# Performance work log

Hardware: AMD Instinct MI355X
Metric: run time of the kernel (lower is better)

## Reference

```python
import jax, jax.numpy as jnp
import numpy as np

I_SZ, H_SZ, B, T = 256, 512, 32, 2048


def _lin_params(key, fan_in, out):
    kw, kb = jax.random.split(key)
    s = 1.0 / np.sqrt(fan_in)
    W = jax.random.uniform(kw, (out, fan_in), minval=-s, maxval=s, dtype=jnp.float32)
    b = jax.random.uniform(kb, (out,), minval=-s, maxval=s, dtype=jnp.float32)
    return W, b


def setup_inputs() -> dict:
    key = jax.random.key(0)
    ks = jax.random.split(key, 11)
    inp = {
        'x': jax.random.normal(ks[0], (B, T, I_SZ), dtype=jnp.float32),
        'hx': jax.random.normal(ks[1], (B, H_SZ), dtype=jnp.float32),
        'cx': jax.random.normal(ks[2], (B, H_SZ), dtype=jnp.float32),
    }
    names_in = ['Wii', 'Wif', 'Wic', 'Wio']
    names_h = ['Whi', 'Whf', 'Whc', 'Who']
    for i, n in enumerate(names_in):
        W, b = _lin_params(ks[3 + i], I_SZ, H_SZ)
        inp[n] = W
        inp['b' + n[1:]] = b
    for i, n in enumerate(names_h):
        W, b = _lin_params(ks[7 + i], H_SZ, H_SZ)
        inp[n] = W
        inp['b' + n[1:]] = b
    return inp


def reference(x, hx, cx, Wii, bii, Wif, bif, Wic, bic, Wio, bio,
              Whi, bhi, Whf, bhf, Whc, bhc, Who, bho):
    # batch_first: [B,T,I] -> [T,B,I]
    xs = jnp.swapaxes(x, 0, 1)
    t, b, _ = xs.shape
    # Fuse the 4 input-to-hidden projections over the whole sequence (same math)
    xi = jnp.einsum('tbi,hi->tbh', xs, Wii) + bii
    xf = jnp.einsum('tbi,hi->tbh', xs, Wif) + bif
    xc = jnp.einsum('tbi,hi->tbh', xs, Wic) + bic
    xo = jnp.einsum('tbi,hi->tbh', xs, Wio) + bio

    def step(carry, gates_x):
        h, c, _, _, _ = carry
        xi_t, xf_t, xc_t, xo_t = gates_x
        ig = jax.nn.sigmoid(xi_t + h @ Whi.T + bhi)
        fg = jax.nn.sigmoid(xf_t + h @ Whf.T + bhf)
        cg = jnp.tanh(xc_t + h @ Whc.T + bhc)
        og = jax.nn.sigmoid(xo_t + h @ Who.T + bho)
        cy = fg * c + ig * cg
        hy = og * jnp.tanh(cy)
        return (hy, cy, ig, fg, og), hy

    z = jnp.zeros((b, H_SZ), dtype=x.dtype)
    (hn, cn, ig_n, fg_n, og_n), ys = jax.lax.scan(
        step, (hx, cx, z, z, z), (xi, xf, xc, xo))
    # torch.cat(list of [B,H], dim=0) -> [T*B, H]; then transpose(0,1) -> [H, T*B]
    out = ys.reshape(t * b, H_SZ).T
    return (out, hn, cn, ig_n, fg_n, og_n)
```

## Files before the change

### kernel.cpp

```cpp
#include <hip/hip_runtime.h>
#include <hip/hip_bf16.h>


typedef _Float16 f16x8 __attribute__((ext_vector_type(8)));
typedef float    f32x16 __attribute__((ext_vector_type(16)));

#define NBLK   32
#define TSTEPS 2048

#define WS_WH    0
#define WS_WX    2097152
#define WS_XG    3145728
#define WS_HG    36700160
#define WS_BIAS  36765696
#define WS_CNT   36773888

#define OUT_MAIN 33554432
#define OFF_HN   (OUT_MAIN)
#define OFF_CN   (OUT_MAIN + 16384)
#define OFF_IG   (OUT_MAIN + 32768)
#define OFF_FG   (OUT_MAIN + 49152)
#define OFF_OG   (OUT_MAIN + 65536)

struct Ptrs { const float* p[16]; };

__device__ __forceinline__ float sigf(float v) {
    return 1.0f / (1.0f + __expf(-v));
}
__device__ __forceinline__ float tanhf_(float v) {
    float a = fabsf(v);
    float e = __expf(-2.0f * a);
    float r = (1.0f - e) / (1.0f + e);
    return v < 0.0f ? -r : r;
}

__global__ void setup_kernel(Ptrs P, const float* __restrict__ hx,
                             _Float16* __restrict__ WH16, _Float16* __restrict__ WX16,
                             float* __restrict__ BIAS, _Float16* __restrict__ HG,
                             unsigned* __restrict__ CNT)
{
    int idx = blockIdx.x * 256 + threadIdx.x;
    if (idx < 1048576) {
        int g = idx >> 18; int r = idx & 262143;
        WH16[idx] = (_Float16)P.p[8 + 2*g][r];
    } else if (idx < 1572864) {
        int j = idx - 1048576; int g = j >> 17; int r = j & 131071;
        WX16[j] = (_Float16)P.p[2*g][r];
    } else if (idx < 1574912) {
        int j = idx - 1572864; int g = j >> 9; int c = j & 511;
        BIAS[j] = P.p[2*g + 1][c] + P.p[8 + 2*g + 1][c];
    } else if (idx < 1576960) {
        int ch = idx - 1574912;
        int kf = ch >> 6; int lane = ch & 63;
        int b = lane & 31; int k0 = (kf*2 + (lane >> 5)) * 8;
        f16x8 o;
        #pragma unroll
        for (int e = 0; e < 8; ++e) o[e] = (_Float16)hx[b*512 + k0 + e];
        *(f16x8*)(HG + (size_t)ch * 8) = o;
    } else if (idx == 1576960) {
        *CNT = 0u;
    }
}

__global__ void xconv_kernel(const float* __restrict__ x, _Float16* __restrict__ XG)
{
    int ch = blockIdx.x * 256 + threadIdx.x;
    int t = ch >> 10; int rest = ch & 1023;
    int kf = rest >> 6; int lane = rest & 63;
    int b = lane & 31; int i0 = (kf*2 + (lane >> 5)) * 8;
    const float* src = x + ((size_t)b * 2048 + t) * 256 + i0;
    float4 u = *(const float4*)src;
    float4 v = *(const float4*)(src + 4);
    f16x8 o;
    o[0]=(_Float16)u.x; o[1]=(_Float16)u.y; o[2]=(_Float16)u.z; o[3]=(_Float16)u.w;
    o[4]=(_Float16)v.x; o[5]=(_Float16)v.y; o[6]=(_Float16)v.z; o[7]=(_Float16)v.w;
    *(f16x8*)(XG + (size_t)ch * 8) = o;
}

__global__ __launch_bounds__(256, 1) void lstm_rec(
    const float* __restrict__ cx, float* __restrict__ out,
    const _Float16* __restrict__ WH16, const _Float16* __restrict__ WX16,
    const _Float16* __restrict__ XG, _Float16* __restrict__ HG,
    const float* __restrict__ BIAS, unsigned* __restrict__ CNT)
{
    __shared__ float part[2][32][66];
    __shared__ float bias_lds[4][16];

    const int tid = threadIdx.x;
    const int bk  = blockIdx.x;
    const int jbase = bk * 16;
    const int w  = tid >> 6;
    const int l  = tid & 63;
    const int kh = w & 1;
    const int cs = w >> 1;
    const int n  = l & 31;
    const int kg = l >> 5;

    if (tid < 64) bias_lds[tid >> 4][tid & 15] = BIAS[(tid >> 4)*512 + jbase + (tid & 15)];

    const int c_loc = cs*32 + n;
    const int g  = c_loc >> 4;
    const int jr = jbase + (c_loc & 15);

    f16x8 bf[24];
    #pragma unroll
    for (int m = 0; m < 16; ++m) {
        int k = (kh*16 + m)*16 + kg*8;
        bf[m] = *(const f16x8*)(WH16 + ((size_t)g*512 + jr)*512 + k);
    }
    #pragma unroll
    for (int m = 0; m < 8; ++m) {
        int i = (kh*8 + m)*16 + kg*8;
        bf[16 + m] = *(const f16x8*)(WX16 + ((size_t)g*512 + jr)*256 + i);
    }

    const int eb = tid & 31;
    const int ej = tid >> 5;
    float c0 = cx[eb*512 + jbase + ej];
    float c1 = cx[eb*512 + jbase + ej + 8];

    __syncthreads();

    for (int t = 0; t < TSTEPS; ++t) {
        const _Float16* hcur = HG + (size_t)(t & 1) * 16384;

        f16x8 ah[16], ax[8];
        #pragma unroll
        for (int m = 0; m < 8; ++m)
            ax[m] = *(const f16x8*)(XG + (size_t)t*8192 + (size_t)(kh*8 + m)*512 + l*8);
        #pragma unroll
        for (int m = 0; m < 16; ++m)
            ah[m] = *(const f16x8*)(hcur + (size_t)(kh*16 + m)*512 + l*8);

        f32x16 accA, accB;
        #pragma unroll
        for (int i = 0; i < 16; ++i) { accA[i] = 0.0f; accB[i] = 0.0f; }

        #pragma unroll
        for (int m = 0; m < 8; m += 2) {
            accA = __builtin_amdgcn_mfma_f32_32x32x16_f16(ax[m],   bf[16+m],   accA, 0, 0, 0);
            accB = __builtin_amdgcn_mfma_f32_32x32x16_f16(ax[m+1], bf[16+m+1], accB, 0, 0, 0);
        }
        #pragma unroll
        for (int m = 0; m < 16; m += 2) {
            accA = __builtin_amdgcn_mfma_f32_32x32x16_f16(ah[m],   bf[m],   accA, 0, 0, 0);
            accB = __builtin_amdgcn_mfma_f32_32x32x16_f16(ah[m+1], bf[m+1], accB, 0, 0, 0);
        }

        #pragma unroll
        for (int r = 0; r < 16; ++r) {
            int b = (r & 3) + 8*(r >> 2) + 4*kg;
            part[kh][b][c_loc] = accA[r] + accB[r];
        }
        __syncthreads();

        _Float16* hnxt = HG + (size_t)((t + 1) & 1) * 16384;
        float hy0, hy1;
        {
            float v0 = part[0][eb][ 0 + ej] + part[1][eb][ 0 + ej] + bias_lds[0][ej];
            float v1 = part[0][eb][16 + ej] + part[1][eb][16 + ej] + bias_lds[1][ej];
            float v2 = part[0][eb][32 + ej] + part[1][eb][32 + ej] + bias_lds[2][ej];
            float v3 = part[0][eb][48 + ej] + part[1][eb][48 + ej] + bias_lds[3][ej];
            float ig = sigf(v0), fg = sigf(v1), cg = tanhf_(v2), og = sigf(v3);
            c0 = fg*c0 + ig*cg;
            hy0 = og * tanhf_(c0);
            if (t == TSTEPS - 1) {
                int k = jbase + ej;
                out[OFF_HN + eb*512 + k] = hy0;
                out[OFF_CN + eb*512 + k] = c0;
                out[OFF_IG + eb*512 + k] = ig;
                out[OFF_FG + eb*512 + k] = fg;
                out[OFF_OG + eb*512 + k] = og;
            }
        }
        {
            int ej2 = ej + 8;
            float v0 = part[0][eb][ 0 + ej2] + part[1][eb][ 0 + ej2] + bias_lds[0][ej2];
            float v1 = part[0][eb][16 + ej2] + part[1][eb][16 + ej2] + bias_lds[1][ej2];
            float v2 = part[0][eb][32 + ej2] + part[1][eb][32 + ej2] + bias_lds[2][ej2];
            float v3 = part[0][eb][48 + ej2] + part[1][eb][48 + ej2] + bias_lds[3][ej2];
            float ig = sigf(v0), fg = sigf(v1), cg = tanhf_(v2), og = sigf(v3);
            c1 = fg*c1 + ig*cg;
            hy1 = og * tanhf_(c1);
            if (t == TSTEPS - 1) {
                int k = jbase + ej2;
                out[OFF_HN + eb*512 + k] = hy1;
                out[OFF_CN + eb*512 + k] = c1;
                out[OFF_IG + eb*512 + k] = ig;
                out[OFF_FG + eb*512 + k] = fg;
                out[OFF_OG + eb*512 + k] = og;
            }
        }

        out[(size_t)(jbase + ej)     * 65536 + t*32 + eb] = hy0;
        out[(size_t)(jbase + ej + 8) * 65536 + t*32 + eb] = hy1;

        {
            int k  = jbase + ej;
            hnxt[bk*512 + eb*8 + ej]        = (_Float16)hy0;
            hnxt[bk*512 + (32 + eb)*8 + ej] = (_Float16)hy1;
            (void)k;
        }

        __syncthreads();
        if (tid == 0) {
            __threadfence();
            __hip_atomic_fetch_add(CNT, 1u, __ATOMIC_RELAXED, __HIP_MEMORY_SCOPE_AGENT);
            const unsigned tgt = (unsigned)NBLK * (unsigned)(t + 1);
            while (__hip_atomic_load(CNT, __ATOMIC_RELAXED, __HIP_MEMORY_SCOPE_AGENT) < tgt) {
                __builtin_amdgcn_s_sleep(1);
            }
            __threadfence();
        }
        __syncthreads();
    }
}

extern "C" void kernel_launch(void* const* d_in, const int* in_sizes, int n_in,
                              void* d_out, int out_size, void* d_ws, size_t ws_size,
                              hipStream_t stream)
{
    const float* x  = (const float*)d_in[0];
    const float* hx = (const float*)d_in[1];
    const float* cx = (const float*)d_in[2];

    Ptrs P;
    for (int i = 0; i < 16; ++i) P.p[i] = (const float*)d_in[3 + i];

    char* ws = (char*)d_ws;
    _Float16* WH16 = (_Float16*)(ws + WS_WH);
    _Float16* WX16 = (_Float16*)(ws + WS_WX);
    _Float16* XG   = (_Float16*)(ws + WS_XG);
    _Float16* HG   = (_Float16*)(ws + WS_HG);
    float*    BIAS = (float*)   (ws + WS_BIAS);
    unsigned* CNT  = (unsigned*)(ws + WS_CNT);

    float* out = (float*)d_out;

    setup_kernel<<<6161, 256, 0, stream>>>(P, hx, WH16, WX16, BIAS, HG, CNT);
    xconv_kernel<<<8192, 256, 0, stream>>>(x, XG);
    lstm_rec<<<NBLK, 256, 0, stream>>>(cx, out, WH16, WX16, XG, HG, BIAS, CNT);
}
```

Before: 12.97 ms.

## Replace atomic-counter grid barrier with per-block flags and overlap x-projection

Swaps the single global atomic counter barrier for per-block step flags. Each block publishes its step number after writing h, and a single wave polls all 32 flags before reading h. The input-projection MFMAs now run before the wait, and the h-vector and global output stores move after the flag publish so they overlap with other blocks' progress. h is written as packed half2 atomic stores with a changed column assignment. Correctness relies on relaxed atomics plus an explicit vmcnt wait instead of threadfences, which risks memory-ordering subtleties.

```diff
diff --git a/kernel.cpp b/kernel.cpp
--- a/kernel.cpp
+++ b/kernel.cpp
@@ -13,7 +13,7 @@
 #define WS_XG    3145728
 #define WS_HG    36700160
 #define WS_BIAS  36765696
-#define WS_CNT   36773888
+#define WS_FLG   36773888
 
 #define OUT_MAIN 33554432
 #define OFF_HN   (OUT_MAIN)
@@ -37,7 +37,7 @@
 __global__ void setup_kernel(Ptrs P, const float* __restrict__ hx,
                              _Float16* __restrict__ WH16, _Float16* __restrict__ WX16,
                              float* __restrict__ BIAS, _Float16* __restrict__ HG,
-                             unsigned* __restrict__ CNT)
+                             unsigned* __restrict__ FLAGS)
 {
     int idx = blockIdx.x * 256 + threadIdx.x;
     if (idx < 1048576) {
@@ -57,8 +57,8 @@
         #pragma unroll
         for (int e = 0; e < 8; ++e) o[e] = (_Float16)hx[b*512 + k0 + e];
         *(f16x8*)(HG + (size_t)ch * 8) = o;
-    } else if (idx == 1576960) {
-        *CNT = 0u;
+    } else if (idx < 1576992) {
+        FLAGS[idx - 1576960] = 0u;
     }
 }
 
@@ -81,7 +81,7 @@
     const float* __restrict__ cx, float* __restrict__ out,
     const _Float16* __restrict__ WH16, const _Float16* __restrict__ WX16,
     const _Float16* __restrict__ XG, _Float16* __restrict__ HG,
-    const float* __restrict__ BIAS, unsigned* __restrict__ CNT)
+    const float* __restrict__ BIAS, unsigned* __restrict__ FLAGS)
 {
     __shared__ float part[2][32][66];
     __shared__ float bias_lds[4][16];
@@ -115,22 +115,18 @@
     }
 
     const int eb = tid & 31;
-    const int ej = tid >> 5;
-    float c0 = cx[eb*512 + jbase + ej];
-    float c1 = cx[eb*512 + jbase + ej + 8];
+    const int ep = tid >> 5;
+    float c0 = cx[eb*512 + jbase + 2*ep];
+    float c1 = cx[eb*512 + jbase + 2*ep + 1];
+    const int hdw = bk*256 + (ep < 4 ? (eb*4 + ep) : ((32 + eb)*4 + (ep - 4)));
 
     __syncthreads();
 
     for (int t = 0; t < TSTEPS; ++t) {
-        const _Float16* hcur = HG + (size_t)(t & 1) * 16384;
-
-        f16x8 ah[16], ax[8];
+        f16x8 ax[8];
         #pragma unroll
         for (int m = 0; m < 8; ++m)
             ax[m] = *(const f16x8*)(XG + (size_t)t*8192 + (size_t)(kh*8 + m)*512 + l*8);
-        #pragma unroll
-        for (int m = 0; m < 16; ++m)
-            ah[m] = *(const f16x8*)(hcur + (size_t)(kh*16 + m)*512 + l*8);
 
         f32x16 accA, accB;
         #pragma unroll
@@ -141,6 +137,28 @@
             accA = __builtin_amdgcn_mfma_f32_32x32x16_f16(ax[m],   bf[16+m],   accA, 0, 0, 0);
             accB = __builtin_amdgcn_mfma_f32_32x32x16_f16(ax[m+1], bf[16+m+1], accB, 0, 0, 0);
         }
+
+        if (w == 0) {
+            for (;;) {
+                unsigned v = __hip_atomic_load(FLAGS + (l & 31), __ATOMIC_RELAXED,
+                                               __HIP_MEMORY_SCOPE_AGENT);
+                if (__all((int)(v >= (unsigned)t))) break;
+                __builtin_amdgcn_s_sleep(1);
+            }
+        }
+        __syncthreads();
+
+        const unsigned long long* hcur64 =
+            (const unsigned long long*)HG + (size_t)(t & 1) * 4096;
+        f16x8 ah[16];
+        #pragma unroll
+        for (int m = 0; m < 16; ++m) {
+            int bofs = ((kh*16 + m)*64 + l) * 2;
+            union { f16x8 v; unsigned long long u[2]; } tq;
+            tq.u[0] = __hip_atomic_load(hcur64 + bofs,     __ATOMIC_RELAXED, __HIP_MEMORY_SCOPE_AGENT);
+            tq.u[1] = __hip_atomic_load(hcur64 + bofs + 1, __ATOMIC_RELAXED, __HIP_MEMORY_SCOPE_AGENT);
+            ah[m] = tq.v;
+        }
         #pragma unroll
         for (int m = 0; m < 16; m += 2) {
             accA = __builtin_amdgcn_mfma_f32_32x32x16_f16(ah[m],   bf[m],   accA, 0, 0, 0);
@@ -154,65 +172,50 @@
         }
         __syncthreads();
 
-        _Float16* hnxt = HG + (size_t)((t + 1) & 1) * 16384;
-        float hy0, hy1;
+        const int ca = 2*ep, cb = 2*ep + 1;
+        float hy0, hy1, ig0, fg0, og0, ig1, fg1, og1;
         {
-            float v0 = part[0][eb][ 0 + ej] + part[1][eb][ 0 + ej] + bias_lds[0][ej];
-            float v1 = part[0][eb][16 + ej] + part[1][eb][16 + ej] + bias_lds[1][ej];
-            float v2 = part[0][eb][32 + ej] + part[1][eb][32 + ej] + bias_lds[2][ej];
-            float v3 = part[0][eb][48 + ej] + part[1][eb][48 + ej] + bias_lds[3][ej];
-            float ig = sigf(v0), fg = sigf(v1), cg = tanhf_(v2), og = sigf(v3);
-            c0 = fg*c0 + ig*cg;
-            hy0 = og * tanhf_(c0);
-            if (t == TSTEPS - 1) {
-                int k = jbase + ej;
-                out[OFF_HN + eb*512 + k] = hy0;
-                out[OFF_CN + eb*512 + k] = c0;
-                out[OFF_IG + eb*512 + k] = ig;
-                out[OFF_FG + eb*512 + k] = fg;
-                out[OFF_OG + eb*512 + k] = og;
-            }
+            float v0 = part[0][eb][ 0 + ca] + part[1][eb][ 0 + ca] + bias_lds[0][ca];
+            float v1 = part[0][eb][16 + ca] + part[1][eb][16 + ca] + bias_lds[1][ca];
+            float v2 = part[0][eb][32 + ca] + part[1][eb][32 + ca] + bias_lds[2][ca];
+            float v3 = part[0][eb][48 + ca] + part[1][eb][48 + ca] + bias_lds[3][ca];
+            ig0 = sigf(v0); fg0 = sigf(v1); float cg = tanhf_(v2); og0 = sigf(v3);
+            c0 = fg0*c0 + ig0*cg;
+            hy0 = og0 * tanhf_(c0);
         }
         {
-            int ej2 = ej + 8;
-            float v0 = part[0][eb][ 0 + ej2] + part[1][eb][ 0 + ej2] + bias_lds[0][ej2];
-            float v1 = part[0][eb][16 + ej2] + part[1][eb][16 + ej2] + bias_lds[1][ej2];
-            float v2 = part[0][eb][32 + ej2] + part[1][eb][32 + ej2] + bias_lds[2][ej2];
-            float v3 = part[0][eb][48 + ej2] + part[1][eb][48 + ej2] + bias_lds[3][ej2];
-            float ig = sigf(v0), fg = sigf(v1), cg = tanhf_(v2), og = sigf(v3);
-            c1 = fg*c1 + ig*cg;
-            hy1 = og * tanhf_(c1);
-            if (t == TSTEPS - 1) {
-                int k = jbase + ej2;
-                out[OFF_HN + eb*512 + k] = hy1;
-                out[OFF_CN + eb*512 + k] = c1;
-                out[OFF_IG + eb*512 + k] = ig;
-                out[OFF_FG + eb*512 + k] = fg;
-                out[OFF_OG + eb*512 + k] = og;
-            }
-        }
-
-        out[(size_t)(jbase + ej)     * 65536 + t*32 + eb] = hy0;
-        out[(size_t)(jbase + ej + 8) * 65536 + t*32 + eb] = hy1;
+            float v0 = part[0][eb][ 0 + cb] + part[1][eb][ 0 + cb] + bias_lds[0][cb];
+            float v1 = part[0][eb][16 + cb] + part[1][eb][16 + cb] + bias_lds[1][cb];
+            float v2 = part[0][eb][32 + cb] + part[1][eb][32 + cb] + bias_lds[2][cb];
+            float v3 = part[0][eb][48 + cb] + part[1][eb][48 + cb] + bias_lds[3][cb];
+            ig1 = sigf(v0); fg1 = sigf(v1); float cg = tanhf_(v2); og1 = sigf(v3);
+            c1 = fg1*c1 + ig1*cg;
+            hy1 = og1 * tanhf_(c1);
+        }
 
         {
-            int k  = jbase + ej;
-            hnxt[bk*512 + eb*8 + ej]        = (_Float16)hy0;
-            hnxt[bk*512 + (32 + eb)*8 + ej] = (_Float16)hy1;
-            (void)k;
-        }
-
+            union { unsigned u; _Float16 h[2]; } pk;
+            pk.h[0] = (_Float16)hy0; pk.h[1] = (_Float16)hy1;
+            unsigned* hnxt32 = (unsigned*)HG + (size_t)((t + 1) & 1) * 8192;
+            __hip_atomic_store(hnxt32 + hdw, pk.u, __ATOMIC_RELAXED,
+                               __HIP_MEMORY_SCOPE_AGENT);
+        }
+        asm volatile("s_waitcnt vmcnt(0)" ::: "memory");
         __syncthreads();
-        if (tid == 0) {
-            __threadfence();
-            __hip_atomic_fetch_add(CNT, 1u, __ATOMIC_RELAXED, __HIP_MEMORY_SCOPE_AGENT);
-            const unsigned tgt = (unsigned)NBLK * (unsigned)(t + 1);
-            while (__hip_atomic_load(CNT, __ATOMIC_RELAXED, __HIP_MEMORY_SCOPE_AGENT) < tgt) {
-                __builtin_amdgcn_s_sleep(1);
-            }
-            __threadfence();
-        }
-        __syncthreads();
+        if (tid == 0)
+            __hip_atomic_store(FLAGS + bk, (unsigned)(t + 1), __ATOMIC_RELAXED,
+                               __HIP_MEMORY_SCOPE_AGENT);
+
+        out[(size_t)(jbase + ca) * 65536 + t*32 + eb] = hy0;
+        out[(size_t)(jbase + cb) * 65536 + t*32 + eb] = hy1;
+        if (t == TSTEPS - 1) {
+            int k0 = jbase + ca, k1 = jbase + cb;
+            out[OFF_HN + eb*512 + k0] = hy0;  out[OFF_HN + eb*512 + k1] = hy1;
+            out[OFF_CN + eb*512 + k0] = c0;   out[OFF_CN + eb*512 + k1] = c1;
+            out[OFF_IG + eb*512 + k0] = ig0;  out[OFF_IG + eb*512 + k1] = ig1;
+            out[OFF_FG + eb*512 + k0] = fg0;  out[OFF_FG + eb*512 + k1] = fg1;
+            out[OFF_OG + eb*512 + k0] = og0;  out[OFF_OG + eb*512 + k1] = og1;
+        }
     }
 }
 
@@ -233,11 +236,11 @@
     _Float16* XG   = (_Float16*)(ws + WS_XG);
     _Float16* HG   = (_Float16*)(ws + WS_HG);
     float*    BIAS = (float*)   (ws + WS_BIAS);
-    unsigned* CNT  = (unsigned*)(ws + WS_CNT);
+    unsigned* FLAGS= (unsigned*)(ws + WS_FLG);
 
     float* out = (float*)d_out;
 
-    setup_kernel<<<6161, 256, 0, stream>>>(P, hx, WH16, WX16, BIAS, HG, CNT);
+    setup_kernel<<<6161, 256, 0, stream>>>(P, hx, WH16, WX16, BIAS, HG, FLAGS);
     xconv_kernel<<<8192, 256, 0, stream>>>(x, XG);
-    lstm_rec<<<NBLK, 256, 0, stream>>>(cx, out, WH16, WX16, XG, HG, BIAS, CNT);
-}
+    lstm_rec<<<NBLK, 256, 0, stream>>>(cx, out, WH16, WX16, XG, HG, BIAS, FLAGS);
+}
```

New measurement: 12.13 ms. 1.07x faster.
